# Performance work log

Hardware: AMD Instinct MI355X
Metric: run time of the kernel (lower is better)

## Reference

```python
import jax, jax.numpy as jnp
import numpy as np

B, L, N, F = 8, 4096, 128, 128          # batch, pixels (64x64), memories, filters
H, DK, DV = 8, 16, 32                   # heads, key dim/head, value dim/head
TK, TV = H * DK, H * DV                 # total key depth 128, total value depth 256
BOT, FFN = 256, 2048                    # bottleneck (2*filters), feed-forward channels
EPS = 1e-3                              # keras BatchNormalization epsilon
INV = float(1.0 / np.sqrt(1.0 + EPS))   # inference BN with moving mean=0, var=1


def _bn_pair(k, shape):
    kg, kb = jax.random.split(k)
    gamma = jax.random.uniform(kg, shape, jnp.float32, 0.5, 1.5)
    beta = 0.1 * jax.random.normal(kb, shape, jnp.float32)
    return jnp.stack([gamma, beta])


def setup_inputs() -> dict:
    key = jax.random.key(0)
    ks = jax.random.split(key, 24)
    s = float(BOT) ** -0.5  # TruncatedNormal(stddev=bottleneck**-0.5) init for qkv convs
    return {
        "pixel_input": jax.random.normal(ks[0], (B, L, F), jnp.float32),
        "memory_input": jax.random.normal(ks[1], (B, N, F), jnp.float32),
        "W_mem1": 0.05 * jax.random.normal(ks[2], (F, BOT), jnp.float32),
        "bn_mem1": _bn_pair(ks[3], (BOT,)),
        "W_pix1": 0.05 * jax.random.normal(ks[4], (F, BOT), jnp.float32),
        "bn_pix1": _bn_pair(ks[5], (BOT,)),
        "W_mem_qkv": s * jax.random.normal(ks[6], (BOT, 2 * TK + TV), jnp.float32),
        "bn_mem_qkv": _bn_pair(ks[7], (2 * TK + TV,)),
        "W_pix_qkv": s * jax.random.normal(ks[8], (BOT, 2 * TK + TV), jnp.float32),
        "bn_pix_qkv": _bn_pair(ks[9], (2 * TK + TV,)),
        "bn_mem_sim": _bn_pair(ks[10], (H,)),
        "bn_mem_ret": _bn_pair(ks[11], (H, DV)),
        "bn_pix_sim": _bn_pair(ks[12], (H,)),
        "bn_pix_ret": _bn_pair(ks[13], (H, DV)),
        "W_mem3": 0.05 * jax.random.normal(ks[14], (TV, F), jnp.float32),
        "bn_mem3": _bn_pair(ks[15], (F,)),
        "W_pix3": 0.05 * jax.random.normal(ks[16], (TV, F), jnp.float32),
        "bn_pix3": _bn_pair(ks[17], (F,)),
        "W_ffn1": 0.05 * jax.random.normal(ks[18], (F, FFN), jnp.float32),
        "bn_ffn1": _bn_pair(ks[19], (FFN,)),
        "W_ffn2": 0.05 * jax.random.normal(ks[20], (FFN, F), jnp.float32),
        "bn_ffn2": _bn_pair(ks[21], (F,)),
    }


def _cbn(x, W, p, relu=False):
    """Conv1D (kernel=1) + inference BatchNorm over channels (+ optional relu)."""
    y = jnp.einsum('blc,cd->bld', x, W)
    y = y * (p[0] * INV) + p[1]
    return jax.nn.relu(y) if relu else y


def _heads(t, d):
    b, l, _ = t.shape  # [b, l, H*d] -> [b, H, l, d]
    return t.reshape(b, l, H, d).transpose(0, 2, 1, 3)


def reference(pixel_input, memory_input, W_mem1, bn_mem1, W_pix1, bn_pix1,
              W_mem_qkv, bn_mem_qkv, W_pix_qkv, bn_pix_qkv,
              bn_mem_sim, bn_mem_ret, bn_pix_sim, bn_pix_ret,
              W_mem3, bn_mem3, W_pix3, bn_pix3,
              W_ffn1, bn_ffn1, W_ffn2, bn_ffn2):
    # Bottleneck projections (conv1 + BN + relu)
    mem = _cbn(memory_input, W_mem1, bn_mem1, True)   # [B, N, BOT]
    pix = _cbn(pixel_input, W_pix1, bn_pix1, True)    # [B, L, BOT]

    # QKV projections (conv + BN, no activation)
    mqkv = _cbn(mem, W_mem_qkv, bn_mem_qkv)           # [B, N, 2*TK+TV]
    pqkv = _cbn(pix, W_pix_qkv, bn_pix_qkv)           # [B, L, 2*TK+TV]
    mq, mk, mv = mqkv[..., :TK], mqkv[..., TK:2 * TK], mqkv[..., 2 * TK:]
    pq, pk, pv = pqkv[..., :TK], pqkv[..., TK:2 * TK], pqkv[..., 2 * TK:]
    mq_h, mk_h = _heads(mq, DK), _heads(mk, DK)       # [B, H, N, DK]
    pq_h, pk_h = _heads(pq, DK), _heads(pk, DK)       # [B, H, L, DK]
    mv_h = mv.reshape(B, N, H, DV)                    # [B, N, H, DV]
    pv_h = pv.reshape(B, L, H, DV)                    # [B, L, H, DV]

    # Memory path: memory2pixel attention + memory self-attention share softmax
    k_cat = jnp.concatenate([pk_h, mk_h], axis=2)     # [B, H, L+N, DK]
    v_cat = jnp.concatenate([pv_h, mv_h], axis=1)     # [B, L+N, H, DV]
    logits = jnp.einsum('bhnd,bhmd->bhnm', mq_h, k_cat)
    logits = logits * (bn_mem_sim[0] * INV)[None, :, None, None] + bn_mem_sim[1][None, :, None, None]
    attn = jax.nn.softmax(logits, axis=-1)
    ret = jnp.einsum('bhnm,bmhd->bhnd', attn, v_cat)  # [B, H, N, DV]
    ret = ret * (bn_mem_ret[0] * INV)[None, :, None, :] + bn_mem_ret[1][None, :, None, :]
    ret = jax.nn.relu(ret).transpose(0, 2, 1, 3).reshape(B, N, TV)
    mem_out = jax.nn.relu(memory_input + _cbn(ret, W_mem3, bn_mem3))
    ffn = _cbn(mem_out, W_ffn1, bn_ffn1, True)
    mem_out = jax.nn.relu(mem_out + _cbn(ffn, W_ffn2, bn_ffn2))

    # Pixel path: pixel2memory feedback attention (sigmoid activation)
    plogits = jnp.einsum('bhld,bhnd->bhln', pq_h, mk_h)
    plogits = plogits * (bn_pix_sim[0] * INV)[None, :, None, None] + bn_pix_sim[1][None, :, None, None]
    pattn = jax.nn.sigmoid(plogits)
    pret = jnp.einsum('bhln,bnhd->bhld', pattn, mv_h)  # [B, H, L, DV]
    pret = pret * (bn_pix_ret[0] * INV)[None, :, None, :] + bn_pix_ret[1][None, :, None, :]
    pret = jax.nn.relu(pret).transpose(0, 2, 1, 3).reshape(B, L, TV)
    pix_out = jax.nn.relu(pixel_input + _cbn(pret, W_pix3, bn_pix3))

    return pix_out, mem_out
```

## Files before the change

kernel.cpp:

```cpp
#include <hip/hip_runtime.h>

typedef __attribute__((ext_vector_type(8))) short short8;
typedef __attribute__((ext_vector_type(4))) float floatx4;

#define INVC 0.9995003746877732f
#define NCHUNK 33

__device__ __forceinline__ unsigned short f2bf(float f) {
    union { float f; unsigned int u; } c; c.f = f;
    unsigned int r = c.u + 0x7fffu + ((c.u >> 16) & 1u);
    return (unsigned short)(r >> 16);
}
__device__ __forceinline__ float bf2f(unsigned short u) {
    union { unsigned int u; float f; } c; c.u = ((unsigned int)u) << 16;
    return c.f;
}
__device__ __forceinline__ void gld_lds16(const unsigned short* g, unsigned short* l) {
    __builtin_amdgcn_global_load_lds(
        (const __attribute__((address_space(1))) unsigned int*)g,
        (__attribute__((address_space(3))) unsigned int*)l, 16, 0, 0);
}
__device__ __forceinline__ int fidx(int row, int k) {
    return (k >> 5) * 512 + (row + 16 * ((k >> 3) & 3)) * 8 + (k & 7);
}

struct PrepPtrs {
    const float* src_pix;
    unsigned short* dst_pix;
    const float* W[8]; unsigned short* Wt[8];
};

__global__ __launch_bounds__(256) void prep_kernel(PrepPtrs P) {
    __shared__ float T[32][33];
    const int bid = blockIdx.x, t = threadIdx.x;
    if (bid < 4096) {
        int i = bid * 1024 + t * 4;
        float4 v = *(const float4*)(P.src_pix + i);
        unsigned long long pk = (unsigned long long)f2bf(v.x)
            | ((unsigned long long)f2bf(v.y) << 16)
            | ((unsigned long long)f2bf(v.z) << 32)
            | ((unsigned long long)f2bf(v.w) << 48);
        *(unsigned long long*)(P.dst_pix + i) = pk;
        return;
    }
    int rel = bid - 4096;
    const int KD[8]  = {128,128,256,256,256,256,128,2048};
    const int ND[8]  = {256,256,512,512,128,128,2048,128};
    const int CNT[8] = {32,32,128,128,32,32,256,256};
    int wi = 0;
    #pragma unroll
    for (int k = 0; k < 8; ++k) { if (rel >= CNT[k] && wi == k) { rel -= CNT[k]; wi = k + 1; } }
    const int K = KD[wi], N = ND[wi];
    const int ntn = N >> 5;
    const int tn = rel % ntn, tk = rel / ntn;
    const int n0 = tn * 32, k0 = tk * 32;
    const float* W = P.W[wi];
    unsigned short* Wt = P.Wt[wi];
    const int tx = t & 31, ty = t >> 5;
    #pragma unroll
    for (int i = 0; i < 4; ++i)
        T[ty + 8*i][tx] = W[(size_t)(k0 + ty + 8*i) * N + n0 + tx];
    __syncthreads();
    #pragma unroll
    for (int i = 0; i < 4; ++i)
        Wt[(size_t)(n0 + ty + 8*i) * K + k0 + tx] = f2bf(T[tx][ty + 8*i]);
}

__device__ __forceinline__ void gemm_body(
    const unsigned short* __restrict__ A,
    const unsigned short* __restrict__ Bt,
    const float* __restrict__ bnp,
    const float* __restrict__ residF,
    unsigned short* __restrict__ outB,
    float* __restrict__ outF,
    int K, int Nc, int do_relu, int row0, int col0,
    unsigned short* As, unsigned short* Bs)
{
    const int t = threadIdx.x;
    const int lane = t & 63, w = t >> 6;
    const int l15 = lane & 15, quad = lane >> 4;
    const int wr = w >> 1, wc = w & 1;

    floatx4 acc[4][4];
    #pragma unroll
    for (int i = 0; i < 4; ++i)
        #pragma unroll
        for (int j = 0; j < 4; ++j) acc[i][j] = (floatx4){0.f, 0.f, 0.f, 0.f};

    const unsigned short* gA0 = A  + (size_t)(row0 + w*16     + l15) * K + quad*8;
    const unsigned short* gA1 = A  + (size_t)(row0 + (w+4)*16 + l15) * K + quad*8;
    const unsigned short* gB0 = Bt + (size_t)(col0 + w*16     + l15) * K + quad*8;
    const unsigned short* gB1 = Bt + (size_t)(col0 + (w+4)*16 + l15) * K + quad*8;
    unsigned short* lA0 = &As[w * 512];
    unsigned short* lA1 = &As[(w + 4) * 512];
    unsigned short* lB0 = &Bs[w * 512];
    unsigned short* lB1 = &Bs[(w + 4) * 512];

    for (int k0 = 0; k0 < K; k0 += 32) {
        __syncthreads();
        gld_lds16(gA0 + k0, lA0);
        gld_lds16(gA1 + k0, lA1);
        gld_lds16(gB0 + k0, lB0);
        gld_lds16(gB1 + k0, lB1);
        __syncthreads();
        short8 a[4], b[4];
        #pragma unroll
        for (int mt = 0; mt < 4; ++mt) a[mt] = *(const short8*)&As[(wr*4 + mt)*512 + lane*8];
        #pragma unroll
        for (int nt = 0; nt < 4; ++nt) b[nt] = *(const short8*)&Bs[(wc*4 + nt)*512 + lane*8];
        #pragma unroll
        for (int mt = 0; mt < 4; ++mt)
            #pragma unroll
            for (int nt = 0; nt < 4; ++nt)
                acc[mt][nt] = __builtin_amdgcn_mfma_f32_16x16x32_bf16(a[mt], b[nt], acc[mt][nt], 0, 0, 0);
    }

    #pragma unroll
    for (int mt = 0; mt < 4; ++mt) {
        const int rowb = row0 + wr*64 + mt*16 + quad*4;
        #pragma unroll
        for (int nt = 0; nt < 4; ++nt) {
            const int col = col0 + wc*64 + nt*16 + l15;
            floatx4 v = acc[mt][nt];
            const float g  = bnp[col] * INVC;
            const float be = bnp[Nc + col];
            #pragma unroll
            for (int r = 0; r < 4; ++r) {
                size_t off = (size_t)(rowb + r) * Nc + col;
                float v1 = v[r] * g + be;
                if (residF) v1 += residF[off];
                if (do_relu) v1 = fmaxf(v1, 0.f);
                if (outB) outB[off] = f2bf(v1);
                if (outF) outF[off] = v1;
            }
        }
    }
}

__global__ __launch_bounds__(256, 4) void gemm_bf16(
    const unsigned short* __restrict__ A, const unsigned short* __restrict__ Bt,
    const float* __restrict__ bnp, unsigned short* __restrict__ outB,
    int K, int Nc)
{
    __shared__ unsigned short As[8 * 512];
    __shared__ unsigned short Bs[8 * 512];
    gemm_body(A, Bt, bnp, nullptr, outB, nullptr, K, Nc, 0,
              blockIdx.y * 128, blockIdx.x * 128, As, Bs);
}

__global__ __launch_bounds__(256) void k_pix1_memfused(
    const unsigned short* __restrict__ pixB, const unsigned short* __restrict__ Wt1,
    const float* __restrict__ bn_pix1, unsigned short* __restrict__ pixA,
    const float* __restrict__ memory_input,
    const unsigned short* __restrict__ Wt0, const float* __restrict__ bn1,
    const unsigned short* __restrict__ Wt2, const float* __restrict__ bnq,
    unsigned short* __restrict__ mqkv)
{
    __shared__ unsigned short As[8 * 512];
    __shared__ unsigned short Bs[8 * 512];
    const int bx = blockIdx.x;
    if (bx < 512) {
        gemm_body(pixB, Wt1, bn_pix1, nullptr, pixA, nullptr, 128, 256, 1,
                  (bx >> 1) * 128, (bx & 1) * 128, As, Bs);
        return;
    }
    unsigned short* A0 = As;
    unsigned short* A1 = Bs;
    const int t = threadIdx.x;
    const int lane = t & 63, w = t >> 6;
    const int l15 = lane & 15, quad = lane >> 4;
    const int g0 = (bx - 512) * 16;

    {
        const int row = t >> 4;
        const int c0 = (t & 15) * 8;
        const float* src = memory_input + (size_t)(g0 + row) * 128 + c0;
        float4 v0 = *(const float4*)src;
        float4 v1 = *(const float4*)(src + 4);
        float vv[8] = {v0.x, v0.y, v0.z, v0.w, v1.x, v1.y, v1.z, v1.w};
        #pragma unroll
        for (int e = 0; e < 8; ++e)
            A0[fidx(row, c0 + e)] = f2bf(vv[e]);
    }
    __syncthreads();

    #pragma unroll
    for (int i = 0; i < 4; ++i) {
        const int n0 = (w*4 + i) * 16;
        floatx4 acc = {0.f,0.f,0.f,0.f};
        #pragma unroll
        for (int kc = 0; kc < 4; ++kc) {
            short8 a = *(const short8*)&A0[kc*512 + lane*8];
            short8 bfr = *(const short8*)&Wt0[(size_t)(n0 + l15)*128 + kc*32 + quad*8];
            acc = __builtin_amdgcn_mfma_f32_16x16x32_bf16(a, bfr, acc, 0, 0, 0);
        }
        const int col = n0 + l15;
        const float g = bn1[col] * INVC, be = bn1[256 + col];
        #pragma unroll
        for (int r = 0; r < 4; ++r) {
            const int row = quad*4 + r;
            float v = fmaxf(acc[r]*g + be, 0.f);
            A1[fidx(row, col)] = f2bf(v);
        }
    }
    __syncthreads();

    #pragma unroll
    for (int i = 0; i < 8; ++i) {
        const int n0 = w*128 + i*16;
        floatx4 acc = {0.f,0.f,0.f,0.f};
        #pragma unroll
        for (int kc = 0; kc < 8; ++kc) {
            short8 a = *(const short8*)&A1[kc*512 + lane*8];
            short8 bfr = *(const short8*)&Wt2[(size_t)(n0 + l15)*256 + kc*32 + quad*8];
            acc = __builtin_amdgcn_mfma_f32_16x16x32_bf16(a, bfr, acc, 0, 0, 0);
        }
        const int col = n0 + l15;
        const float g = bnq[col] * INVC, be = bnq[512 + col];
        #pragma unroll
        for (int r = 0; r < 4; ++r) {
            const int row = quad*4 + r;
            mqkv[(size_t)(g0 + row)*512 + col] = f2bf(acc[r]*g + be);
        }
    }
}

__global__ __launch_bounds__(256, 4) void k_attn(
    const unsigned short* __restrict__ pqkv,
    const unsigned short* __restrict__ mqkv,
    const float* __restrict__ bn_psim, const float* __restrict__ bn_pret,
    unsigned short* __restrict__ pret,
    const float* __restrict__ bn_msim,
    float* __restrict__ part_acc, float* __restrict__ part_ml)
{
    __shared__ unsigned short Qs[4*512];
    __shared__ unsigned short Ks[8*512];
    __shared__ unsigned short VsT[8*512];
    __shared__ unsigned short Ps[16*512];
    const int t = threadIdx.x;
    const int lane = t & 63, w = t >> 6;
    const int l15 = lane & 15, quad = lane >> 4;
    floatx4 z4 = {0.f, 0.f, 0.f, 0.f};
    const uint4 zz = make_uint4(0u,0u,0u,0u);

    const int is_pix = (blockIdx.x < 4096);
    int b, h, qrow0;
    const unsigned short* kvbase;
    if (is_pix) {
        const int bx = blockIdx.x;
        const int lt = bx & 63; h = (bx >> 6) & 7; b = bx >> 9;
        qrow0 = b*4096 + lt*64;
        kvbase = mqkv + ((size_t)(b*128) << 9);
    } else {
        const int bxm = blockIdx.x - 4096;
        const int c = bxm % NCHUNK;
        const int rest = bxm / NCHUNK;
        const int qh = rest & 1; h = (rest >> 1) & 7; b = rest >> 4;
        qrow0 = b*128 + qh*64;
        kvbase = (c < 32) ? (pqkv + ((size_t)(b*4096 + c*128) << 9))
                          : (mqkv + ((size_t)(b*128) << 9));
    }
    const unsigned short* qbase = is_pix ? pqkv : mqkv;

    {
        const int r = t >> 1, half = t & 1;
        if (t < 128) {
            const unsigned short* src = qbase + ((size_t)(qrow0 + r) << 9) + h*16 + half*8;
            *(uint4*)&Qs[(r>>4)*512 + ((r&15) + 16*half)*8] = *(const uint4*)src;
            *(uint4*)&Qs[(r>>4)*512 + ((r&15) + 16*(2+half))*8] = zz;
        }
        const unsigned short* ksrc = kvbase + ((size_t)r << 9) + 128 + h*16 + half*8;
        *(uint4*)&Ks[(r>>4)*512 + ((r&15) + 16*half)*8] = *(const uint4*)ksrc;
        *(uint4*)&Ks[(r>>4)*512 + ((r&15) + 16*(2+half))*8] = zz;
        const unsigned short* vsrc = kvbase + ((size_t)r << 9) + 256 + h*32 + half*16;
        uint4 va = *(const uint4*)vsrc;
        uint4 vb = *(const uint4*)(vsrc + 8);
        unsigned short ev[16] = {
            (unsigned short)(va.x & 0xffffu), (unsigned short)(va.x >> 16),
            (unsigned short)(va.y & 0xffffu), (unsigned short)(va.y >> 16),
            (unsigned short)(va.z & 0xffffu), (unsigned short)(va.z >> 16),
            (unsigned short)(va.w & 0xffffu), (unsigned short)(va.w >> 16),
            (unsigned short)(vb.x & 0xffffu), (unsigned short)(vb.x >> 16),
            (unsigned short)(vb.y & 0xffffu), (unsigned short)(vb.y >> 16),
            (unsigned short)(vb.z & 0xffffu), (unsigned short)(vb.z >> 16),
            (unsigned short)(vb.w & 0xffffu), (unsigned short)(vb.w >> 16)};
        const int vbase_off = (half*4 + (r>>5))*512 + 16*((r>>3)&3)*8 + (r&7);
        #pragma unroll
        for (int e = 0; e < 16; ++e)
            VsT[vbase_off + e*8] = ev[e];
    }
    __syncthreads();

    const float simg = (is_pix ? bn_psim[h] : bn_msim[h]) * INVC;
    const float simb =  is_pix ? bn_psim[8 + h] : bn_msim[8 + h];
    short8 aq = *(const short8*)&Qs[w*512 + lane*8];
    float mx4[4], ls4[4];

    if (is_pix) {
        #pragma unroll
        for (int nt = 0; nt < 8; ++nt) {
            short8 bk = *(const short8*)&Ks[nt*512 + lane*8];
            floatx4 s = __builtin_amdgcn_mfma_f32_16x16x32_bf16(aq, bk, z4, 0, 0, 0);
            const int pbase = (w*4 + (nt>>1))*512 + 16*((nt&1)*2 + (l15>>3))*8 + (l15&7);
            #pragma unroll
            for (int r = 0; r < 4; ++r) {
                float x = s[r] * simg + simb;
                float p = __builtin_amdgcn_rcpf(1.f + __expf(-x));
                Ps[pbase + (quad*4 + r)*8] = f2bf(p);
            }
        }
    } else {
        float sv[8][4];
        #pragma unroll
        for (int nt = 0; nt < 8; ++nt) {
            short8 bk = *(const short8*)&Ks[nt*512 + lane*8];
            floatx4 s = __builtin_amdgcn_mfma_f32_16x16x32_bf16(aq, bk, z4, 0, 0, 0);
            #pragma unroll
            for (int r = 0; r < 4; ++r) sv[nt][r] = s[r] * simg + simb;
        }
        #pragma unroll
        for (int r = 0; r < 4; ++r) {
            float mx = sv[0][r];
            #pragma unroll
            for (int nt = 1; nt < 8; ++nt) mx = fmaxf(mx, sv[nt][r]);
            mx = fmaxf(mx, __shfl_xor(mx, 1));
            mx = fmaxf(mx, __shfl_xor(mx, 2));
            mx = fmaxf(mx, __shfl_xor(mx, 4));
            mx = fmaxf(mx, __shfl_xor(mx, 8));
            float lsum = 0.f;
            #pragma unroll
            for (int nt = 0; nt < 8; ++nt) {
                float p = __expf(sv[nt][r] - mx);
                lsum += p;
                Ps[(w*4 + (nt>>1))*512 + ((quad*4+r) + 16*((nt&1)*2 + (l15>>3)))*8 + (l15&7)] = f2bf(p);
            }
            lsum += __shfl_xor(lsum, 1);
            lsum += __shfl_xor(lsum, 2);
            lsum += __shfl_xor(lsum, 4);
            lsum += __shfl_xor(lsum, 8);
            mx4[r] = mx; ls4[r] = lsum;
        }
    }

    #pragma unroll
    for (int dvt = 0; dvt < 2; ++dvt) {
        floatx4 acc = {0.f,0.f,0.f,0.f};
        #pragma unroll
        for (int ks = 0; ks < 4; ++ks) {
            short8 ap = *(const short8*)&Ps[(w*4 + ks)*512 + lane*8];
            short8 bv = *(const short8*)&VsT[(dvt*4 + ks)*512 + lane*8];
            acc = __builtin_amdgcn_mfma_f32_16x16x32_bf16(ap, bv, acc, 0, 0, 0);
        }
        if (is_pix) {
            const int dv = dvt*16 + l15;
            const float g  = bn_pret[h*32 + dv] * INVC;
            const float be = bn_pret[256 + h*32 + dv];
            #pragma unroll
            for (int r = 0; r < 4; ++r) {
                const int row = qrow0 + w*16 + quad*4 + r;
                float v = fmaxf(acc[r] * g + be, 0.f);
                pret[((size_t)row << 8) + h*32 + dv] = f2bf(v);
            }
        } else {
            const int bxm = blockIdx.x - 4096;
            const int c = bxm % NCHUNK;
            const int rest = bxm / NCHUNK;
            const int qh = rest & 1;
            const int bh = b*8 + h;
            const int dv = dvt*16 + l15;
            #pragma unroll
            for (int r = 0; r < 4; ++r) {
                const int q = qh*64 + w*16 + quad*4 + r;
                part_acc[((size_t)(bh*NCHUNK + c)*128 + q)*32 + dv] = acc[r];
            }
        }
    }
    if (!is_pix && l15 == 0) {
        const int bxm = blockIdx.x - 4096;
        const int c = bxm % NCHUNK;
        const int rest = bxm / NCHUNK;
        const int qh = rest & 1;
        const int bh = b*8 + h;
        #pragma unroll
        for (int r = 0; r < 4; ++r) {
            const int q = qh*64 + w*16 + quad*4 + r;
            size_t o = ((size_t)(bh*NCHUNK + c)*128 + q) * 2;
            part_ml[o]     = mx4[r];
            part_ml[o + 1] = ls4[r];
        }
    }
}

__global__ __launch_bounds__(256) void k_pix3_combmem3(
    const unsigned short* __restrict__ pretB, const unsigned short* __restrict__ Wt5,
    const float* __restrict__ bn_pix3, const float* __restrict__ pixel_input,
    float* __restrict__ out_pix,
    const float* __restrict__ part_acc, const float* __restrict__ part_ml,
    const float* __restrict__ bn_ret,
    const unsigned short* __restrict__ Wt4, const float* __restrict__ bn3,
    const float* __restrict__ memory_input,
    unsigned short* __restrict__ moB)
{
    __shared__ unsigned short As[8 * 512];
    __shared__ unsigned short Bs[8 * 512];
    const int bx = blockIdx.x;
    if (bx < 256) {
        gemm_body(pretB, Wt5, bn_pix3, pixel_input, nullptr, out_pix, 256, 128, 1,
                  bx * 128, 0, As, Bs);
        return;
    }
    unsigned short* mretA = As;
    const int t = threadIdx.x;
    const int lane = t & 63, w = t >> 6;
    const int l15 = lane & 15, quad = lane >> 4;
    const int g0 = (bx - 256) * 16;
    const int b = g0 >> 7;
    const int nbase = g0 & 127;

    {
        const int row = t >> 4;
        const int c0 = (t & 15) * 16;
        const int h = c0 >> 5;
        const int n = nbase + row;
        const int bh = b*8 + h;
        float m_g = -1e30f;
        for (int s = 0; s < NCHUNK; ++s)
            m_g = fmaxf(m_g, part_ml[((size_t)(bh*NCHUNK + s)*128 + n)*2]);
        float l_g = 0.f;
        float og[16];
        #pragma unroll
        for (int e = 0; e < 16; ++e) og[e] = 0.f;
        for (int s = 0; s < NCHUNK; ++s) {
            size_t o = ((size_t)(bh*NCHUNK + s)*128 + n)*2;
            float wgt = __expf(part_ml[o] - m_g);
            l_g += part_ml[o+1] * wgt;
            const float* pa = part_acc + ((size_t)(bh*NCHUNK + s)*128 + n)*32 + (c0 & 31);
            #pragma unroll
            for (int e = 0; e < 16; e += 4) {
                float4 v = *(const float4*)(pa + e);
                og[e]   += v.x*wgt; og[e+1] += v.y*wgt;
                og[e+2] += v.z*wgt; og[e+3] += v.w*wgt;
            }
        }
        float invl = __builtin_amdgcn_rcpf(l_g);
        #pragma unroll
        for (int e = 0; e < 16; ++e) {
            int col = c0 + e;
            int dv = col & 31;
            float v = og[e]*invl*(bn_ret[h*32+dv]*INVC) + bn_ret[256 + h*32 + dv];
            mretA[fidx(row, col)] = f2bf(fmaxf(v, 0.f));
        }
    }
    __syncthreads();

    #pragma unroll
    for (int i = 0; i < 2; ++i) {
        const int n0 = (w*2 + i) * 16;
        floatx4 acc = {0.f,0.f,0.f,0.f};
        #pragma unroll
        for (int kc = 0; kc < 8; ++kc) {
            short8 a = *(const short8*)&mretA[kc*512 + lane*8];
            short8 bfr = *(const short8*)&Wt4[(size_t)(n0 + l15)*256 + kc*32 + quad*8];
            acc = __builtin_amdgcn_mfma_f32_16x16x32_bf16(a, bfr, acc, 0, 0, 0);
        }
        const int col = n0 + l15;
        const float g = bn3[col]*INVC, be = bn3[128 + col];
        #pragma unroll
        for (int r = 0; r < 4; ++r) {
            const int row = quad*4 + r;
            float v = acc[r]*g + be + memory_input[(size_t)(g0 + row)*128 + col];
            moB[(size_t)(g0 + row)*128 + col] = f2bf(fmaxf(v, 0.f));
        }
    }
}

__global__ __launch_bounds__(1024) void k_ffn(
    const unsigned short* __restrict__ moB,
    const unsigned short* __restrict__ Wt6, const float* __restrict__ bnf1,
    const unsigned short* __restrict__ Wt7, const float* __restrict__ bnf2,
    float* __restrict__ out_mem)
{
    __shared__ unsigned short moA[4*512];
    __shared__ unsigned short fA[64*512];
    __shared__ floatx4 red[2][8][64];
    const int t = threadIdx.x;
    const int lane = t & 63, w = t >> 6;
    const int l15 = lane & 15, quad = lane >> 4;
    const int g0 = blockIdx.x * 16;

    if (t < 256) {
        const int row = t >> 4;
        const int c0 = (t & 15) * 8;
        uint4 v = *(const uint4*)(moB + (size_t)(g0 + row)*128 + c0);
        unsigned short e0 = (unsigned short)(v.x & 0xffffu), e1 = (unsigned short)(v.x >> 16);
        unsigned short e2 = (unsigned short)(v.y & 0xffffu), e3 = (unsigned short)(v.y >> 16);
        unsigned short e4 = (unsigned short)(v.z & 0xffffu), e5 = (unsigned short)(v.z >> 16);
        unsigned short e6 = (unsigned short)(v.w & 0xffffu), e7 = (unsigned short)(v.w >> 16);
        moA[fidx(row, c0+0)] = e0; moA[fidx(row, c0+1)] = e1;
        moA[fidx(row, c0+2)] = e2; moA[fidx(row, c0+3)] = e3;
        moA[fidx(row, c0+4)] = e4; moA[fidx(row, c0+5)] = e5;
        moA[fidx(row, c0+6)] = e6; moA[fidx(row, c0+7)] = e7;
    }
    __syncthreads();

    #pragma unroll
    for (int i = 0; i < 8; ++i) {
        const int n0 = (w*8 + i) * 16;
        floatx4 acc = {0.f,0.f,0.f,0.f};
        #pragma unroll
        for (int kc = 0; kc < 4; ++kc) {
            short8 a = *(const short8*)&moA[kc*512 + lane*8];
            short8 bfr = *(const short8*)&Wt6[(size_t)(n0 + l15)*128 + kc*32 + quad*8];
            acc = __builtin_amdgcn_mfma_f32_16x16x32_bf16(a, bfr, acc, 0, 0, 0);
        }
        const int col = n0 + l15;
        const float g = bnf1[col]*INVC, be = bnf1[2048 + col];
        #pragma unroll
        for (int r = 0; r < 4; ++r)
            fA[fidx(quad*4 + r, col)] = f2bf(fmaxf(acc[r]*g + be, 0.f));
    }
    __syncthreads();

    {
        const int ntile = w & 7, khalf = w >> 3;
        const int n0 = ntile * 16;
        floatx4 acc = {0.f,0.f,0.f,0.f};
        #pragma unroll 8
        for (int kc = 0; kc < 32; ++kc) {
            const int kcu = khalf*32 + kc;
            short8 a = *(const short8*)&fA[kcu*512 + lane*8];
            short8 bfr = *(const short8*)&Wt7[(size_t)(n0 + l15)*2048 + kcu*32 + quad*8];
            acc = __builtin_amdgcn_mfma_f32_16x16x32_bf16(a, bfr, acc, 0, 0, 0);
        }
        red[khalf][ntile][lane] = acc;
    }
    __syncthreads();
    if (w < 8) {
        const int n0 = w * 16;
        floatx4 s0 = red[0][w][lane];
        floatx4 s1 = red[1][w][lane];
        const int col = n0 + l15;
        const float g = bnf2[col]*INVC, be = bnf2[128 + col];
        #pragma unroll
        for (int r = 0; r < 4; ++r) {
            const int row = quad*4 + r;
            float resid = bf2f(moA[fidx(row, col)]);
            float v = fmaxf((s0[r] + s1[r])*g + be + resid, 0.f);
            out_mem[(size_t)(g0 + row)*128 + col] = v;
        }
    }
}

extern "C" void kernel_launch(void* const* d_in, const int* in_sizes, int n_in,
                              void* d_out, int out_size, void* d_ws, size_t ws_size,
                              hipStream_t stream) {
    const float* pixel_input  = (const float*)d_in[0];
    const float* memory_input = (const float*)d_in[1];
    const float* W_mem1    = (const float*)d_in[2];
    const float* bn_mem1   = (const float*)d_in[3];
    const float* W_pix1    = (const float*)d_in[4];
    const float* bn_pix1   = (const float*)d_in[5];
    const float* W_mem_qkv = (const float*)d_in[6];
    const float* bn_mem_qkv= (const float*)d_in[7];
    const float* W_pix_qkv = (const float*)d_in[8];
    const float* bn_pix_qkv= (const float*)d_in[9];
    const float* bn_mem_sim= (const float*)d_in[10];
    const float* bn_mem_ret= (const float*)d_in[11];
    const float* bn_pix_sim= (const float*)d_in[12];
    const float* bn_pix_ret= (const float*)d_in[13];
    const float* W_mem3    = (const float*)d_in[14];
    const float* bn_mem3   = (const float*)d_in[15];
    const float* W_pix3    = (const float*)d_in[16];
    const float* bn_pix3   = (const float*)d_in[17];
    const float* W_ffn1    = (const float*)d_in[18];
    const float* bn_ffn1   = (const float*)d_in[19];
    const float* W_ffn2    = (const float*)d_in[20];
    const float* bn_ffn2   = (const float*)d_in[21];

    char* ws = (char*)d_ws;
    size_t off = 0;
    auto alloc = [&](size_t bytes) -> void* {
        void* p = ws + off; off += (bytes + 255) & ~(size_t)255; return p;
    };
    unsigned short* pixB  = (unsigned short*)alloc((size_t)32768*128*2);
    unsigned short* Wt0   = (unsigned short*)alloc((size_t)256*128*2);
    unsigned short* Wt1   = (unsigned short*)alloc((size_t)256*128*2);
    unsigned short* Wt2   = (unsigned short*)alloc((size_t)512*256*2);
    unsigned short* Wt3   = (unsigned short*)alloc((size_t)512*256*2);
    unsigned short* Wt4   = (unsigned short*)alloc((size_t)128*256*2);
    unsigned short* Wt5   = (unsigned short*)alloc((size_t)128*256*2);
    unsigned short* Wt6   = (unsigned short*)alloc((size_t)2048*128*2);
    unsigned short* Wt7   = (unsigned short*)alloc((size_t)128*2048*2);
    unsigned short* mqkvB = (unsigned short*)alloc((size_t)1024*512*2);
    unsigned short* pixA  = (unsigned short*)alloc((size_t)32768*256*2);
    unsigned short* pqkvB = (unsigned short*)alloc((size_t)32768*512*2);
    float* part_acc = (float*)alloc((size_t)64*NCHUNK*128*32*4);
    float* part_ml  = (float*)alloc((size_t)64*NCHUNK*128*2*4);
    unsigned short* pretB = (unsigned short*)alloc((size_t)32768*256*2);
    unsigned short* moB   = (unsigned short*)alloc((size_t)1024*128*2);

    float* out_pix = (float*)d_out;
    float* out_mem = (float*)d_out + (size_t)8*4096*128;

    PrepPtrs P;
    P.src_pix = pixel_input;
    P.dst_pix = pixB;
    P.W[0]=W_mem1; P.W[1]=W_pix1; P.W[2]=W_mem_qkv; P.W[3]=W_pix_qkv;
    P.W[4]=W_mem3; P.W[5]=W_pix3; P.W[6]=W_ffn1;    P.W[7]=W_ffn2;
    P.Wt[0]=Wt0; P.Wt[1]=Wt1; P.Wt[2]=Wt2; P.Wt[3]=Wt3;
    P.Wt[4]=Wt4; P.Wt[5]=Wt5; P.Wt[6]=Wt6; P.Wt[7]=Wt7;

    dim3 blk(256);
    prep_kernel<<<4992, blk, 0, stream>>>(P);
    k_pix1_memfused<<<576, blk, 0, stream>>>(pixB, Wt1, bn_pix1, pixA,
        memory_input, Wt0, bn_mem1, Wt2, bn_mem_qkv, mqkvB);
    gemm_bf16<<<dim3(4,256,1), blk, 0, stream>>>(pixA, Wt3, bn_pix_qkv, pqkvB, 256, 512);
    k_attn<<<4096 + 128*NCHUNK, blk, 0, stream>>>(pqkvB, mqkvB,
        bn_pix_sim, bn_pix_ret, pretB, bn_mem_sim, part_acc, part_ml);
    k_pix3_combmem3<<<320, blk, 0, stream>>>(pretB, Wt5, bn_pix3, pixel_input, out_pix,
        part_acc, part_ml, bn_mem_ret, Wt4, bn_mem3, memory_input, moB);
    k_ffn<<<64, dim3(1024), 0, stream>>>(moB, Wt6, bn_ffn1, Wt7, bn_ffn2, out_mem);
}
```

Measured before the change: 264.3 us.

## Fuse pixel conv1 and QKV GEMMs into one kernel keeping bottleneck in LDS

```diff
diff --git a/kernel.cpp b/kernel.cpp
--- a/kernel.cpp
+++ b/kernel.cpp
@@ -10,6 +10,9 @@
     union { float f; unsigned int u; } c; c.f = f;
     unsigned int r = c.u + 0x7fffu + ((c.u >> 16) & 1u);
     return (unsigned short)(r >> 16);
+}
+__device__ __forceinline__ unsigned int f2bf2(float a, float b) {
+    return (unsigned int)f2bf(a) | ((unsigned int)f2bf(b) << 16);
 }
 __device__ __forceinline__ float bf2f(unsigned short u) {
     union { unsigned int u; float f; } c; c.u = ((unsigned int)u) << 16;
@@ -71,9 +74,8 @@
     const unsigned short* __restrict__ Bt,
     const float* __restrict__ bnp,
     const float* __restrict__ residF,
-    unsigned short* __restrict__ outB,
     float* __restrict__ outF,
-    int K, int Nc, int do_relu, int row0, int col0,
+    int K, int Nc, int row0, int col0,
     unsigned short* As, unsigned short* Bs)
 {
     const int t = threadIdx.x;
@@ -127,50 +129,115 @@
             #pragma unroll
             for (int r = 0; r < 4; ++r) {
                 size_t off = (size_t)(rowb + r) * Nc + col;
-                float v1 = v[r] * g + be;
-                if (residF) v1 += residF[off];
-                if (do_relu) v1 = fmaxf(v1, 0.f);
-                if (outB) outB[off] = f2bf(v1);
-                if (outF) outF[off] = v1;
-            }
-        }
-    }
-}
-
-__global__ __launch_bounds__(256, 4) void gemm_bf16(
-    const unsigned short* __restrict__ A, const unsigned short* __restrict__ Bt,
-    const float* __restrict__ bnp, unsigned short* __restrict__ outB,
-    int K, int Nc)
-{
-    __shared__ unsigned short As[8 * 512];
-    __shared__ unsigned short Bs[8 * 512];
-    gemm_body(A, Bt, bnp, nullptr, outB, nullptr, K, Nc, 0,
-              blockIdx.y * 128, blockIdx.x * 128, As, Bs);
-}
-
-__global__ __launch_bounds__(256) void k_pix1_memfused(
-    const unsigned short* __restrict__ pixB, const unsigned short* __restrict__ Wt1,
-    const float* __restrict__ bn_pix1, unsigned short* __restrict__ pixA,
+                float v1 = v[r] * g + be + residF[off];
+                outF[off] = fmaxf(v1, 0.f);
+            }
+        }
+    }
+}
+
+__global__ __launch_bounds__(256) void k_qkv(
+    const unsigned short* __restrict__ pixB,
+    const unsigned short* __restrict__ Wt1, const float* __restrict__ bn1,
+    const unsigned short* __restrict__ Wt2, const float* __restrict__ bnq,
+    unsigned short* __restrict__ pqkvB,
     const float* __restrict__ memory_input,
-    const unsigned short* __restrict__ Wt0, const float* __restrict__ bn1,
-    const unsigned short* __restrict__ Wt2, const float* __restrict__ bnq,
+    const unsigned short* __restrict__ Wm0, const float* __restrict__ bnm1,
+    const unsigned short* __restrict__ Wm2, const float* __restrict__ bnmq,
     unsigned short* __restrict__ mqkv)
 {
-    __shared__ unsigned short As[8 * 512];
-    __shared__ unsigned short Bs[8 * 512];
-    const int bx = blockIdx.x;
-    if (bx < 512) {
-        gemm_body(pixB, Wt1, bn_pix1, nullptr, pixA, nullptr, 128, 256, 1,
-                  (bx >> 1) * 128, (bx & 1) * 128, As, Bs);
-        return;
-    }
-    unsigned short* A0 = As;
-    unsigned short* A1 = Bs;
+    __shared__ unsigned short A2[64*512];
     const int t = threadIdx.x;
     const int lane = t & 63, w = t >> 6;
     const int l15 = lane & 15, quad = lane >> 4;
-    const int g0 = (bx - 512) * 16;
-
+
+    if (blockIdx.x < 256) {
+        const int row0 = blockIdx.x * 128;
+        short8 afr[4][4];
+        float ga[4][4], ba[4][4];
+        #pragma unroll
+        for (int i = 0; i < 4; ++i) {
+            #pragma unroll
+            for (int kc = 0; kc < 4; ++kc)
+                afr[i][kc] = *(const short8*)&Wt1[(size_t)(w*64 + i*16 + l15)*128 + kc*32 + quad*8];
+            #pragma unroll
+            for (int r = 0; r < 4; ++r) {
+                const int col = w*64 + i*16 + quad*4 + r;
+                ga[i][r] = bn1[col] * INVC;
+                ba[i][r] = bn1[256 + col];
+            }
+        }
+        #pragma unroll
+        for (int ru = 0; ru < 8; ++ru) {
+            short8 bfr[4];
+            #pragma unroll
+            for (int kc = 0; kc < 4; ++kc)
+                bfr[kc] = *(const short8*)&pixB[(size_t)(row0 + ru*16 + l15)*128 + kc*32 + quad*8];
+            #pragma unroll
+            for (int i = 0; i < 4; ++i) {
+                floatx4 acc = {0.f,0.f,0.f,0.f};
+                #pragma unroll
+                for (int kc = 0; kc < 4; ++kc)
+                    acc = __builtin_amdgcn_mfma_f32_16x16x32_bf16(afr[i][kc], bfr[kc], acc, 0, 0, 0);
+                float v[4];
+                #pragma unroll
+                for (int r = 0; r < 4; ++r)
+                    v[r] = fmaxf(acc[r]*ga[i][r] + ba[i][r], 0.f);
+                const int unit = ru*8 + w*2 + (i >> 1);
+                const int koff = (i & 1)*2 + (quad >> 1);
+                const int off  = unit*512 + (l15 + 16*koff)*8 + (quad & 1)*4;
+                uint2 pk; pk.x = f2bf2(v[0], v[1]); pk.y = f2bf2(v[2], v[3]);
+                *(uint2*)&A2[off] = pk;
+            }
+        }
+        __syncthreads();
+
+        #pragma unroll
+        for (int op = 0; op < 4; ++op) {
+            short8 a0[8], a1[8];
+            float g2[2][4], b2[2][4];
+            #pragma unroll
+            for (int kc = 0; kc < 8; ++kc) {
+                a0[kc] = *(const short8*)&Wt2[(size_t)(w*128 + (op*2+0)*16 + l15)*256 + kc*32 + quad*8];
+                a1[kc] = *(const short8*)&Wt2[(size_t)(w*128 + (op*2+1)*16 + l15)*256 + kc*32 + quad*8];
+            }
+            #pragma unroll
+            for (int e = 0; e < 2; ++e)
+                #pragma unroll
+                for (int r = 0; r < 4; ++r) {
+                    const int col = w*128 + (op*2+e)*16 + quad*4 + r;
+                    g2[e][r] = bnq[col] * INVC;
+                    b2[e][r] = bnq[512 + col];
+                }
+            #pragma unroll
+            for (int ru = 0; ru < 8; ++ru) {
+                short8 b[8];
+                #pragma unroll
+                for (int kc = 0; kc < 8; ++kc)
+                    b[kc] = *(const short8*)&A2[(ru*8 + kc)*512 + lane*8];
+                floatx4 acc0 = {0.f,0.f,0.f,0.f}, acc1 = {0.f,0.f,0.f,0.f};
+                #pragma unroll
+                for (int kc = 0; kc < 8; ++kc) {
+                    acc0 = __builtin_amdgcn_mfma_f32_16x16x32_bf16(a0[kc], b[kc], acc0, 0, 0, 0);
+                    acc1 = __builtin_amdgcn_mfma_f32_16x16x32_bf16(a1[kc], b[kc], acc1, 0, 0, 0);
+                }
+                const int row = row0 + ru*16 + l15;
+                unsigned long long pk0 =
+                    (unsigned long long)f2bf2(acc0[0]*g2[0][0]+b2[0][0], acc0[1]*g2[0][1]+b2[0][1])
+                  | ((unsigned long long)f2bf2(acc0[2]*g2[0][2]+b2[0][2], acc0[3]*g2[0][3]+b2[0][3]) << 32);
+                unsigned long long pk1 =
+                    (unsigned long long)f2bf2(acc1[0]*g2[1][0]+b2[1][0], acc1[1]*g2[1][1]+b2[1][1])
+                  | ((unsigned long long)f2bf2(acc1[2]*g2[1][2]+b2[1][2], acc1[3]*g2[1][3]+b2[1][3]) << 32);
+                *(unsigned long long*)&pqkvB[(size_t)row*512 + w*128 + (op*2+0)*16 + quad*4] = pk0;
+                *(unsigned long long*)&pqkvB[(size_t)row*512 + w*128 + (op*2+1)*16 + quad*4] = pk1;
+            }
+        }
+        return;
+    }
+
+    unsigned short* A0 = &A2[0];
+    unsigned short* A1 = &A2[4*512];
+    const int g0 = (blockIdx.x - 256) * 16;
     {
         const int row = t >> 4;
         const int c0 = (t & 15) * 8;
@@ -183,7 +250,6 @@
             A0[fidx(row, c0 + e)] = f2bf(vv[e]);
     }
     __syncthreads();
-
     #pragma unroll
     for (int i = 0; i < 4; ++i) {
         const int n0 = (w*4 + i) * 16;
@@ -191,20 +257,16 @@
         #pragma unroll
         for (int kc = 0; kc < 4; ++kc) {
             short8 a = *(const short8*)&A0[kc*512 + lane*8];
-            short8 bfr = *(const short8*)&Wt0[(size_t)(n0 + l15)*128 + kc*32 + quad*8];
+            short8 bfr = *(const short8*)&Wm0[(size_t)(n0 + l15)*128 + kc*32 + quad*8];
             acc = __builtin_amdgcn_mfma_f32_16x16x32_bf16(a, bfr, acc, 0, 0, 0);
         }
         const int col = n0 + l15;
-        const float g = bn1[col] * INVC, be = bn1[256 + col];
-        #pragma unroll
-        for (int r = 0; r < 4; ++r) {
-            const int row = quad*4 + r;
-            float v = fmaxf(acc[r]*g + be, 0.f);
-            A1[fidx(row, col)] = f2bf(v);
-        }
-    }
-    __syncthreads();
-
+        const float g = bnm1[col] * INVC, be = bnm1[256 + col];
+        #pragma unroll
+        for (int r = 0; r < 4; ++r)
+            A1[fidx(quad*4 + r, col)] = f2bf(fmaxf(acc[r]*g + be, 0.f));
+    }
+    __syncthreads();
     #pragma unroll
     for (int i = 0; i < 8; ++i) {
         const int n0 = w*128 + i*16;
@@ -212,16 +274,14 @@
         #pragma unroll
         for (int kc = 0; kc < 8; ++kc) {
             short8 a = *(const short8*)&A1[kc*512 + lane*8];
-            short8 bfr = *(const short8*)&Wt2[(size_t)(n0 + l15)*256 + kc*32 + quad*8];
+            short8 bfr = *(const short8*)&Wm2[(size_t)(n0 + l15)*256 + kc*32 + quad*8];
             acc = __builtin_amdgcn_mfma_f32_16x16x32_bf16(a, bfr, acc, 0, 0, 0);
         }
         const int col = n0 + l15;
-        const float g = bnq[col] * INVC, be = bnq[512 + col];
-        #pragma unroll
-        for (int r = 0; r < 4; ++r) {
-            const int row = quad*4 + r;
-            mqkv[(size_t)(g0 + row)*512 + col] = f2bf(acc[r]*g + be);
-        }
+        const float g = bnmq[col] * INVC, be = bnmq[512 + col];
+        #pragma unroll
+        for (int r = 0; r < 4; ++r)
+            mqkv[(size_t)(g0 + quad*4 + r)*512 + col] = f2bf(acc[r]*g + be);
     }
 }
 
@@ -244,7 +304,7 @@
     const uint4 zz = make_uint4(0u,0u,0u,0u);
 
     const int is_pix = (blockIdx.x < 4096);
-    int b, h, qrow0;
+    int b, h, qrow0, c = 0, qh = 0;
     const unsigned short* kvbase;
     if (is_pix) {
         const int bx = blockIdx.x;
@@ -253,9 +313,9 @@
         kvbase = mqkv + ((size_t)(b*128) << 9);
     } else {
         const int bxm = blockIdx.x - 4096;
-        const int c = bxm % NCHUNK;
+        c = bxm % NCHUNK;
         const int rest = bxm / NCHUNK;
-        const int qh = rest & 1; h = (rest >> 1) & 7; b = rest >> 4;
+        qh = rest & 1; h = (rest >> 1) & 7; b = rest >> 4;
         qrow0 = b*128 + qh*64;
         kvbase = (c < 32) ? (pqkv + ((size_t)(b*4096 + c*128) << 9))
                           : (mqkv + ((size_t)(b*128) << 9));
@@ -293,53 +353,57 @@
 
     const float simg = (is_pix ? bn_psim[h] : bn_msim[h]) * INVC;
     const float simb =  is_pix ? bn_psim[8 + h] : bn_msim[8 + h];
-    short8 aq = *(const short8*)&Qs[w*512 + lane*8];
-    float mx4[4], ls4[4];
+    short8 bq = *(const short8*)&Qs[w*512 + lane*8];
+    float mstat, lstat;
 
     if (is_pix) {
         #pragma unroll
         for (int nt = 0; nt < 8; ++nt) {
-            short8 bk = *(const short8*)&Ks[nt*512 + lane*8];
-            floatx4 s = __builtin_amdgcn_mfma_f32_16x16x32_bf16(aq, bk, z4, 0, 0, 0);
-            const int pbase = (w*4 + (nt>>1))*512 + 16*((nt&1)*2 + (l15>>3))*8 + (l15&7);
+            short8 ak = *(const short8*)&Ks[nt*512 + lane*8];
+            floatx4 s = __builtin_amdgcn_mfma_f32_16x16x32_bf16(ak, bq, z4, 0, 0, 0);
+            float p[4];
             #pragma unroll
             for (int r = 0; r < 4; ++r) {
                 float x = s[r] * simg + simb;
-                float p = __builtin_amdgcn_rcpf(1.f + __expf(-x));
-                Ps[pbase + (quad*4 + r)*8] = f2bf(p);
-            }
+                p[r] = __builtin_amdgcn_rcpf(1.f + __expf(-x));
+            }
+            const int off = (w*4 + (nt>>1))*512
+                          + (l15 + 16*((nt&1)*2 + (quad>>1)))*8 + (quad&1)*4;
+            uint2 pk; pk.x = f2bf2(p[0], p[1]); pk.y = f2bf2(p[2], p[3]);
+            *(uint2*)&Ps[off] = pk;
         }
     } else {
-        float sv[8][4];
+        floatx4 sv[8];
+        float mx = -1e30f;
         #pragma unroll
         for (int nt = 0; nt < 8; ++nt) {
-            short8 bk = *(const short8*)&Ks[nt*512 + lane*8];
-            floatx4 s = __builtin_amdgcn_mfma_f32_16x16x32_bf16(aq, bk, z4, 0, 0, 0);
-            #pragma unroll
-            for (int r = 0; r < 4; ++r) sv[nt][r] = s[r] * simg + simb;
-        }
-        #pragma unroll
-        for (int r = 0; r < 4; ++r) {
-            float mx = sv[0][r];
-            #pragma unroll
-            for (int nt = 1; nt < 8; ++nt) mx = fmaxf(mx, sv[nt][r]);
-            mx = fmaxf(mx, __shfl_xor(mx, 1));
-            mx = fmaxf(mx, __shfl_xor(mx, 2));
-            mx = fmaxf(mx, __shfl_xor(mx, 4));
-            mx = fmaxf(mx, __shfl_xor(mx, 8));
-            float lsum = 0.f;
-            #pragma unroll
-            for (int nt = 0; nt < 8; ++nt) {
-                float p = __expf(sv[nt][r] - mx);
-                lsum += p;
-                Ps[(w*4 + (nt>>1))*512 + ((quad*4+r) + 16*((nt&1)*2 + (l15>>3)))*8 + (l15&7)] = f2bf(p);
-            }
-            lsum += __shfl_xor(lsum, 1);
-            lsum += __shfl_xor(lsum, 2);
-            lsum += __shfl_xor(lsum, 4);
-            lsum += __shfl_xor(lsum, 8);
-            mx4[r] = mx; ls4[r] = lsum;
-        }
+            short8 ak = *(const short8*)&Ks[nt*512 + lane*8];
+            floatx4 s = __builtin_amdgcn_mfma_f32_16x16x32_bf16(ak, bq, z4, 0, 0, 0);
+            #pragma unroll
+            for (int r = 0; r < 4; ++r) {
+                sv[nt][r] = s[r] * simg + simb;
+                mx = fmaxf(mx, sv[nt][r]);
+            }
+        }
+        mx = fmaxf(mx, __shfl_xor(mx, 16));
+        mx = fmaxf(mx, __shfl_xor(mx, 32));
+        float lsum = 0.f;
+        #pragma unroll
+        for (int nt = 0; nt < 8; ++nt) {
+            float p[4];
+            #pragma unroll
+            for (int r = 0; r < 4; ++r) {
+                p[r] = __expf(sv[nt][r] - mx);
+                lsum += p[r];
+            }
+            const int off = (w*4 + (nt>>1))*512
+                          + (l15 + 16*((nt&1)*2 + (quad>>1)))*8 + (quad&1)*4;
+            uint2 pk; pk.x = f2bf2(p[0], p[1]); pk.y = f2bf2(p[2], p[3]);
+            *(uint2*)&Ps[off] = pk;
+        }
+        lsum += __shfl_xor(lsum, 16);
+        lsum += __shfl_xor(lsum, 32);
+        mstat = mx; lstat = lsum;
     }
 
     #pragma unroll
@@ -347,47 +411,34 @@
         floatx4 acc = {0.f,0.f,0.f,0.f};
         #pragma unroll
         for (int ks = 0; ks < 4; ++ks) {
-            short8 ap = *(const short8*)&Ps[(w*4 + ks)*512 + lane*8];
-            short8 bv = *(const short8*)&VsT[(dvt*4 + ks)*512 + lane*8];
-            acc = __builtin_amdgcn_mfma_f32_16x16x32_bf16(ap, bv, acc, 0, 0, 0);
+            short8 av = *(const short8*)&VsT[(dvt*4 + ks)*512 + lane*8];
+            short8 bp = *(const short8*)&Ps[(w*4 + ks)*512 + lane*8];
+            acc = __builtin_amdgcn_mfma_f32_16x16x32_bf16(av, bp, acc, 0, 0, 0);
         }
         if (is_pix) {
-            const int dv = dvt*16 + l15;
-            const float g  = bn_pret[h*32 + dv] * INVC;
-            const float be = bn_pret[256 + h*32 + dv];
+            const int q = qrow0 + w*16 + l15;
+            float v[4];
             #pragma unroll
             for (int r = 0; r < 4; ++r) {
-                const int row = qrow0 + w*16 + quad*4 + r;
-                float v = fmaxf(acc[r] * g + be, 0.f);
-                pret[((size_t)row << 8) + h*32 + dv] = f2bf(v);
-            }
+                const int dv = dvt*16 + quad*4 + r;
+                v[r] = fmaxf(acc[r] * (bn_pret[h*32 + dv]*INVC) + bn_pret[256 + h*32 + dv], 0.f);
+            }
+            unsigned long long pk = (unsigned long long)f2bf2(v[0], v[1])
+                                  | ((unsigned long long)f2bf2(v[2], v[3]) << 32);
+            *(unsigned long long*)&pret[((size_t)q << 8) + h*32 + dvt*16 + quad*4] = pk;
         } else {
-            const int bxm = blockIdx.x - 4096;
-            const int c = bxm % NCHUNK;
-            const int rest = bxm / NCHUNK;
-            const int qh = rest & 1;
             const int bh = b*8 + h;
-            const int dv = dvt*16 + l15;
-            #pragma unroll
-            for (int r = 0; r < 4; ++r) {
-                const int q = qh*64 + w*16 + quad*4 + r;
-                part_acc[((size_t)(bh*NCHUNK + c)*128 + q)*32 + dv] = acc[r];
-            }
-        }
-    }
-    if (!is_pix && l15 == 0) {
-        const int bxm = blockIdx.x - 4096;
-        const int c = bxm % NCHUNK;
-        const int rest = bxm / NCHUNK;
-        const int qh = rest & 1;
+            const int q = qh*64 + w*16 + l15;
+            float4 st = make_float4(acc[0], acc[1], acc[2], acc[3]);
+            *(float4*)&part_acc[((size_t)(bh*NCHUNK + c)*128 + q)*32 + dvt*16 + quad*4] = st;
+        }
+    }
+    if (!is_pix && quad == 0) {
         const int bh = b*8 + h;
-        #pragma unroll
-        for (int r = 0; r < 4; ++r) {
-            const int q = qh*64 + w*16 + quad*4 + r;
-            size_t o = ((size_t)(bh*NCHUNK + c)*128 + q) * 2;
-            part_ml[o]     = mx4[r];
-            part_ml[o + 1] = ls4[r];
-        }
+        const int q = qh*64 + w*16 + l15;
+        size_t o = ((size_t)(bh*NCHUNK + c)*128 + q) * 2;
+        float2 ml = make_float2(mstat, lstat);
+        *(float2*)&part_ml[o] = ml;
     }
 }
 
@@ -405,7 +456,7 @@
     __shared__ unsigned short Bs[8 * 512];
     const int bx = blockIdx.x;
     if (bx < 256) {
-        gemm_body(pretB, Wt5, bn_pix3, pixel_input, nullptr, out_pix, 256, 128, 1,
+        gemm_body(pretB, Wt5, bn_pix3, pixel_input, out_pix, 256, 128,
                   bx * 128, 0, As, Bs);
         return;
     }
@@ -492,14 +543,13 @@
         const int row = t >> 4;
         const int c0 = (t & 15) * 8;
         uint4 v = *(const uint4*)(moB + (size_t)(g0 + row)*128 + c0);
-        unsigned short e0 = (unsigned short)(v.x & 0xffffu), e1 = (unsigned short)(v.x >> 16);
-        unsigned short e2 = (unsigned short)(v.y & 0xffffu), e3 = (unsigned short)(v.y >> 16);
-        unsigned short e4 = (unsigned short)(v.z & 0xffffu), e5 = (unsigned short)(v.z >> 16);
-        unsigned short e6 = (unsigned short)(v.w & 0xffffu), e7 = (unsigned short)(v.w >> 16);
-        moA[fidx(row, c0+0)] = e0; moA[fidx(row, c0+1)] = e1;
-        moA[fidx(row, c0+2)] = e2; moA[fidx(row, c0+3)] = e3;
-        moA[fidx(row, c0+4)] = e4; moA[fidx(row, c0+5)] = e5;
-        moA[fidx(row, c0+6)] = e6; moA[fidx(row, c0+7)] = e7;
+        unsigned short ev[8] = {
+            (unsigned short)(v.x & 0xffffu), (unsigned short)(v.x >> 16),
+            (unsigned short)(v.y & 0xffffu), (unsigned short)(v.y >> 16),
+            (unsigned short)(v.z & 0xffffu), (unsigned short)(v.z >> 16),
+            (unsigned short)(v.w & 0xffffu), (unsigned short)(v.w >> 16)};
+        #pragma unroll
+        for (int e = 0; e < 8; ++e) moA[fidx(row, c0+e)] = ev[e];
     }
     __syncthreads();
 
@@ -592,7 +642,6 @@
     unsigned short* Wt6   = (unsigned short*)alloc((size_t)2048*128*2);
     unsigned short* Wt7   = (unsigned short*)alloc((size_t)128*2048*2);
     unsigned short* mqkvB = (unsigned short*)alloc((size_t)1024*512*2);
-    unsigned short* pixA  = (unsigned short*)alloc((size_t)32768*256*2);
     unsigned short* pqkvB = (unsigned short*)alloc((size_t)32768*512*2);
     float* part_acc = (float*)alloc((size_t)64*NCHUNK*128*32*4);
     float* part_ml  = (float*)alloc((size_t)64*NCHUNK*128*2*4);
@@ -612,9 +661,8 @@
 
     dim3 blk(256);
     prep_kernel<<<4992, blk, 0, stream>>>(P);
-    k_pix1_memfused<<<576, blk, 0, stream>>>(pixB, Wt1, bn_pix1, pixA,
+    k_qkv<<<320, blk, 0, stream>>>(pixB, Wt1, bn_pix1, Wt3, bn_pix_qkv, pqkvB,
         memory_input, Wt0, bn_mem1, Wt2, bn_mem_qkv, mqkvB);
-    gemm_bf16<<<dim3(4,256,1), blk, 0, stream>>>(pixA, Wt3, bn_pix_qkv, pqkvB, 256, 512);
     k_attn<<<4096 + 128*NCHUNK, blk, 0, stream>>>(pqkvB, mqkvB,
         bn_pix_sim, bn_pix_ret, pretB, bn_mem_sim, part_acc, part_ml);
     k_pix3_combmem3<<<320, blk, 0, stream>>>(pretB, Wt5, bn_pix3, pixel_input, out_pix,
```

New measurement: 238.1 us. 1.11x faster.
